# Kernel tuning notes

Hardware: AMD Instinct MI355X
Metric: run time of the kernel (lower is better)

Reference implementation:

```python
import jax, jax.numpy as jnp
import numpy as np

DN = ('NCHW', 'OIHW', 'NCHW')  # conv dimension numbers
EPS = 1e-5


def _tcn(x, w1, b1, w2, b2, w3, b3):
    """Gated TCN. x: [B,T,N,C] -> [B,T-2,N,Cout].  out = conv1(x)*sigmoid(conv2(x)) + tanh(conv3(x))"""
    xc = jnp.transpose(x, (0, 3, 2, 1))  # [B,C,N,T]
    conv = lambda w, b: jax.lax.conv_general_dilated(xc, w, (1, 1), 'VALID', dimension_numbers=DN) + b[None, :, None, None]
    p = conv(w1, b1)
    q = jax.nn.sigmoid(conv(w2, b2))
    r = jnp.tanh(conv(w3, b3))
    out = p * q + r  # [B,Cout,N,T-2]
    return jnp.transpose(out, (0, 3, 2, 1))


def setup_inputs() -> dict:
    key = jax.random.key(0)
    ks = jax.random.split(key, 16)
    B, T, N, C_in = 32, 24, 1024, 1
    K, C_t, C_s = 3, 64, 16
    inp = {}
    inp['x'] = jax.random.normal(ks[0], (B, T, N, C_in), jnp.float32)
    # stacked Chebyshev polynomials T_0..T_{K-1}, scaled so matmul output stays O(1)
    inp['cheb'] = jax.random.normal(ks[1], (K, N, N), jnp.float32) * (N ** -0.5)
    # temporal conv 1 (C_in -> C_t), kernel (1,3)
    s1 = (2.0 / (C_in * 3 + C_t * 3)) ** 0.5
    for i, nm in enumerate(['t1_w1', 't1_w2', 't1_w3']):
        inp[nm] = jax.random.normal(ks[2 + i], (C_t, C_in, 1, 3), jnp.float32) * s1
        inp[nm.replace('w', 'b')] = jnp.zeros((C_t,), jnp.float32)
    # Chebyshev weights (K, C_t, C_s), xavier-normal
    sc = (2.0 / (C_t + C_s)) ** 0.5
    inp['w_cheb'] = jax.random.normal(ks[5], (K, C_t, C_s), jnp.float32) * sc
    inp['b_cheb'] = jnp.zeros((C_s,), jnp.float32)
    # temporal conv 2 (C_s -> C_s)
    s2 = (2.0 / (C_s * 3 + C_s * 3)) ** 0.5
    for i, nm in enumerate(['t2_w1', 't2_w2', 't2_w3']):
        inp[nm] = jax.random.normal(ks[6 + i], (C_s, C_s, 1, 3), jnp.float32) * s2
        inp[nm.replace('w', 'b')] = jnp.zeros((C_s,), jnp.float32)
    # BatchNorm2d over num_nodes channel
    inp['bn_gamma'] = jnp.ones((N,), jnp.float32)
    inp['bn_beta'] = jnp.zeros((N,), jnp.float32)
    return inp


def reference(x, cheb, t1_w1, t1_b1, t1_w2, t1_b2, t1_w3, t1_b3,
              w_cheb, b_cheb, t2_w1, t2_b1, t2_w2, t2_b2, t2_w3, t2_b3,
              bn_gamma, bn_beta):
    # gated TCN 1: [B,24,N,1] -> [B,22,N,64]
    h = _tcn(x, t1_w1, t1_b1, t1_w2, t1_b2, t1_w3, t1_b3)
    # Chebyshev graph conv fused over all time steps and K taps:
    # T_k_x[b,t,n,c] = sum_m h[b,t,m,c] * cheb[k,m,n]; out = sum_k T_k_x @ W[k]
    s = jnp.einsum('btmc,kmn,kco->btno', h, cheb, w_cheb) + b_cheb  # [B,22,N,16]
    # gated TCN 2: -> [B,20,N,16]
    h2 = _tcn(s, t2_w1, t2_b1, t2_w2, t2_b2, t2_w3, t2_b3)
    # BatchNorm2d over node dim (training-mode batch stats), matching permute(0,2,1,3)
    y = jnp.transpose(h2, (0, 2, 1, 3))  # [B,N,T',C]
    mean = jnp.mean(y, axis=(0, 2, 3), keepdims=True)
    var = jnp.var(y, axis=(0, 2, 3), keepdims=True)  # biased, like torch BN
    y = (y - mean) * jax.lax.rsqrt(var + EPS) * bn_gamma[None, :, None, None] + bn_beta[None, :, None, None]
    y = jnp.transpose(y, (0, 2, 1, 3))  # [B,T',N,C]
    return jax.nn.relu(y)
```

## Files before the change

kernel.cpp:

```cpp
#include <hip/hip_runtime.h>
#include <hip/hip_bf16.h>

using bf16x8 = __attribute__((ext_vector_type(8))) short;
using bf16x4 = __attribute__((ext_vector_type(4))) short;
using f32x4  = __attribute__((ext_vector_type(4))) float;
using f32x2  = __attribute__((ext_vector_type(2))) float;

static __device__ __forceinline__ float bf2f(short s) {
  union { unsigned u; float f; } z;
  z.u = ((unsigned)(unsigned short)s) << 16;
  return z.f;
}
static __device__ __forceinline__ short f2bfs(float f) {
  union { __hip_bfloat16 h; short s; } u;
  u.h = __float2bfloat16(f);
  return u.s;
}
static __device__ __forceinline__ float frcp(float x) { return __builtin_amdgcn_rcpf(x); }
static __device__ __forceinline__ float sigm_f(float x) { return frcp(1.f + __expf(-x)); }
static __device__ __forceinline__ float tanh_f(float x) {
  return fmaf(2.f, frcp(1.f + __expf(-2.f * x)), -1.f);
}

typedef const __attribute__((address_space(1))) unsigned int* gas_u32;
typedef __attribute__((address_space(3))) unsigned int* las_u32;
#define GLOAD16(gp, lp) __builtin_amdgcn_global_load_lds( \
    (gas_u32)(const void*)(gp), (las_u32)(void*)(lp), 16, 0, 0)

__global__ void __launch_bounds__(256) k_front(
    const float* __restrict__ x,
    const float* __restrict__ w1, const float* __restrict__ b1,
    const float* __restrict__ w2, const float* __restrict__ b2,
    const float* __restrict__ w3, const float* __restrict__ b3,
    const float* __restrict__ wcheb,
    __hip_bfloat16* __restrict__ hwt, int bt0, int ch,
    const float* __restrict__ cheb, __hip_bfloat16* __restrict__ chebT) {
  __shared__ __align__(16) char smem[32768];
  const int tid = threadIdx.x;

  if ((int)blockIdx.x >= ch * 4) {
    float (*tile)[65] = reinterpret_cast<float (*)[65]>(smem);
    int blk = blockIdx.x - ch * 4;
    int k = blk >> 8;
    int rem = blk & 255;
    int m0 = (rem >> 4) << 6;
    int n0 = (rem & 15) << 6;
    int tx = tid & 63;
    int ty = tid >> 6;
    const float* src = cheb + (size_t)k * 1024 * 1024;
    #pragma unroll
    for (int i = 0; i < 16; i++) {
      int ml = ty + i * 4;
      tile[ml][tx] = src[(size_t)(m0 + ml) * 1024 + n0 + tx];
    }
    __syncthreads();
    #pragma unroll
    for (int i = 0; i < 16; i++) {
      int nl = ty + i * 4;
      chebT[(size_t)(n0 + nl) * 3072 + k * 1024 + m0 + tx] =
          __float2bfloat16(tile[tx][nl]);
    }
    return;
  }

  char* hls = smem;
  const int lane = tid & 63, w = tid >> 6;
  const int r16 = lane & 15, kb = lane >> 4;
  const int btl = blockIdx.x >> 2;
  const int m0 = (blockIdx.x & 3) << 8;
  const int bt = bt0 + btl;
  const int b = bt / 22, t = bt % 22;

  const float* xp = x + (size_t)(b * 24 + t) * 1024 + m0 + tid;
  const float x0 = xp[0], x1 = xp[1024], x2 = xp[2048];
  const f32x2 x0v = {x0, x0}, x1v = {x1, x1}, x2v = {x2, x2};

  bf16x8 bw[3][2];
  #pragma unroll
  for (int kk = 0; kk < 3; kk++)
    #pragma unroll
    for (int ks = 0; ks < 2; ks++)
      #pragma unroll
      for (int jj = 0; jj < 8; jj++)
        bw[kk][ks][jj] = f2bfs(wcheb[kk * 1024 + (ks * 32 + kb * 8 + jj) * 16 + r16]);

  const int rswz = (tid & 7) << 4;
  #pragma unroll
  for (int cg = 0; cg < 8; cg++) {
    bf16x8 hv;
    #pragma unroll
    for (int j2 = 0; j2 < 4; j2++) {
      const int c2 = cg * 4 + j2;
      const int wi = 6 * c2;
      f32x2 pw = {b1[2*c2], b1[2*c2+1]};
      f32x2 qw = {b2[2*c2], b2[2*c2+1]};
      f32x2 rw = {b3[2*c2], b3[2*c2+1]};
      pw = __builtin_elementwise_fma(x0v, (f32x2){w1[wi], w1[wi+3]}, pw);
      qw = __builtin_elementwise_fma(x0v, (f32x2){w2[wi], w2[wi+3]}, qw);
      rw = __builtin_elementwise_fma(x0v, (f32x2){w3[wi], w3[wi+3]}, rw);
      pw = __builtin_elementwise_fma(x1v, (f32x2){w1[wi+1], w1[wi+4]}, pw);
      qw = __builtin_elementwise_fma(x1v, (f32x2){w2[wi+1], w2[wi+4]}, qw);
      rw = __builtin_elementwise_fma(x1v, (f32x2){w3[wi+1], w3[wi+4]}, rw);
      pw = __builtin_elementwise_fma(x2v, (f32x2){w1[wi+2], w1[wi+5]}, pw);
      qw = __builtin_elementwise_fma(x2v, (f32x2){w2[wi+2], w2[wi+5]}, qw);
      rw = __builtin_elementwise_fma(x2v, (f32x2){w3[wi+2], w3[wi+5]}, rw);
      hv[j2*2+0] = f2bfs(fmaf(pw.x, sigm_f(qw.x), tanh_f(rw.x)));
      hv[j2*2+1] = f2bfs(fmaf(pw.y, sigm_f(qw.y), tanh_f(rw.y)));
    }
    *(bf16x8*)(hls + tid * 128 + ((cg << 4) ^ rswz)) = hv;
  }
  __syncthreads();

  const char* Ab = hls + (w * 64 + r16) * 128;
  const int axor = (r16 & 7) << 4;
  f32x4 acc[4][3];
  #pragma unroll
  for (int mt = 0; mt < 4; mt++)
    #pragma unroll
    for (int kk = 0; kk < 3; kk++) acc[mt][kk] = (f32x4){0.f, 0.f, 0.f, 0.f};

  #pragma unroll
  for (int ks = 0; ks < 2; ks++) {
    #pragma unroll
    for (int mt = 0; mt < 4; mt++) {
      bf16x8 a = *(const bf16x8*)(Ab + mt * 2048 + ((((ks << 2) + kb) << 4) ^ axor));
      #pragma unroll
      for (int kk = 0; kk < 3; kk++)
        acc[mt][kk] = __builtin_amdgcn_mfma_f32_16x16x32_bf16(a, bw[kk][ks], acc[mt][kk], 0, 0, 0);
    }
  }

  __hip_bfloat16* hp = hwt + (size_t)btl * 49152 + r16 * 3072 + m0 + w * 64;
  #pragma unroll
  for (int kk = 0; kk < 3; kk++)
    #pragma unroll
    for (int mt = 0; mt < 4; mt++) {
      bf16x4 v;
      #pragma unroll
      for (int r = 0; r < 4; r++) v[r] = f2bfs(acc[mt][kk][r]);
      *(bf16x4*)(hp + kk * 1024 + mt * 16 + kb * 4) = v;
    }
}

__global__ void __launch_bounds__(256, 2) k_gemm(
    const __hip_bfloat16* __restrict__ chebT,
    const __hip_bfloat16* __restrict__ hwt,
    const float* __restrict__ b_cheb,
    __hip_bfloat16* __restrict__ sbuf,
    int bt_base) {
  __shared__ __align__(16) char smem[32768];
  const int tid = threadIdx.x;
  const int lane = tid & 63;
  const int w = tid >> 6;

  int nt, ct;
  if (gridDim.x == 704) {
    const int xcd = blockIdx.x & 7;
    const int idx = blockIdx.x >> 3;
    nt = ((xcd >> 2) << 2) + (idx & 3);
    ct = (xcd & 3) * 22 + (idx >> 2);
  } else {
    nt = blockIdx.x & 7;
    ct = blockIdx.x >> 3;
  }

  const int srow = tid >> 3;
  const int sswz = ((tid & 7) ^ (srow & 7)) << 4;
  const char* Ag = (const char*)chebT + (size_t)(nt * 128 + srow) * 6144 + sswz;
  const int btl = srow >> 4, so = srow & 15;
  const char* Bg = (const char*)hwt + (size_t)(ct * 8 + btl) * 98304 + (size_t)so * 6144 + sswz;
  char* Als = smem + w * 1024;
  char* Bls = smem + 16384 + w * 1024;

  const int r16 = lane & 15;
  const int c16 = lane >> 4;
  const int wr = (w >> 1) << 6;
  const int wc = (w & 1) << 6;
  const int axor = (r16 & 7) << 4;
  const char* Abase = smem + (wr + r16) * 128;
  const char* Bbase = smem + 16384 + (wc + r16) * 128;

  f32x4 acc[4][4];
  #pragma unroll
  for (int i = 0; i < 4; i++)
    #pragma unroll
    for (int j = 0; j < 4; j++) acc[i][j] = (f32x4){0.f, 0.f, 0.f, 0.f};

  for (int kt = 0; kt < 48; kt++) {
    __syncthreads();
    const char* a = Ag + kt * 128;
    const char* b = Bg + kt * 128;
    #pragma unroll
    for (int i = 0; i < 4; i++) GLOAD16(a + i * 196608, Als + i * 4096);
    #pragma unroll
    for (int i = 0; i < 4; i++) GLOAD16(b + i * 196608, Bls + i * 4096);
    __syncthreads();
    #pragma unroll
    for (int ksub = 0; ksub < 2; ksub++) {
      const int ko = (ksub * 64 + c16 * 16) ^ axor;
      bf16x8 af[4], bfr[4];
      #pragma unroll
      for (int i = 0; i < 4; i++) af[i] = *(const bf16x8*)(Abase + i * 2048 + ko);
      #pragma unroll
      for (int j = 0; j < 4; j++) bfr[j] = *(const bf16x8*)(Bbase + j * 2048 + ko);
      #pragma unroll
      for (int i = 0; i < 4; i++)
        #pragma unroll
        for (int j = 0; j < 4; j++)
          acc[i][j] = __builtin_amdgcn_mfma_f32_16x16x32_bf16(af[i], bfr[j], acc[i][j], 0, 0, 0);
    }
  }

  float bias = b_cheb[r16];
  #pragma unroll
  for (int j = 0; j < 4; j++) {
    int gcol = ct * 128 + wc + j * 16 + r16;
    size_t bt_g = (size_t)bt_base + (gcol >> 4);
    int o = gcol & 15;
    #pragma unroll
    for (int i = 0; i < 4; i++) {
      int n0 = nt * 128 + wr + i * 16 + c16 * 4;
      __hip_bfloat16* sp = sbuf + (bt_g * 1024 + n0) * 16 + o;
      #pragma unroll
      for (int r = 0; r < 4; r++)
        sp[r * 16] = __float2bfloat16(acc[i][j][r] + bias);
    }
  }
}

__global__ void __launch_bounds__(256) k_tcn2(
    const __hip_bfloat16* __restrict__ sbuf,
    const float* __restrict__ w1, const float* __restrict__ b1,
    const float* __restrict__ w2, const float* __restrict__ b2,
    const float* __restrict__ w3, const float* __restrict__ b3,
    __hip_bfloat16* __restrict__ h2b) {
  const int tid = threadIdx.x;
  const int lane = tid & 63, w = tid >> 6;
  const int r16 = lane & 15, kb = lane >> 4;
  const int half = blockIdx.x & 1;
  const int bt2 = blockIdx.x >> 1;
  const int b = bt2 / 20, t2 = bt2 % 20;

  bf16x8 bw[3][2];
  const float* wps[3] = {w1, w2, w3};
  #pragma unroll
  for (int c = 0; c < 3; c++) {
    #pragma unroll
    for (int jj = 0; jj < 8; jj++) {
      int k = kb * 8 + jj;
      bw[c][0][jj] = f2bfs(wps[c][r16 * 48 + (k & 15) * 3 + (k >> 4)]);
      bw[c][1][jj] = (kb < 2) ? f2bfs(wps[c][r16 * 48 + (kb * 8 + jj) * 3 + 2]) : (short)0;
    }
  }
  const float bp = b1[r16], bq = b2[r16], br = b3[r16];

  const char* sb = (const char*)sbuf;
  const size_t slice = (size_t)1024 * 32;
  const int rowbase = half * 512 + w * 128;
  const char* baseA = sb + (size_t)(b * 22 + t2 + (kb >> 1)) * slice
                      + (size_t)(rowbase + r16) * 32 + (kb & 1) * 16;
  const char* baseC = sb + (size_t)(b * 22 + t2 + 2) * slice
                      + (size_t)(rowbase + r16) * 32 + (kb & 1) * 16;
  __hip_bfloat16* outp = h2b + ((size_t)bt2 * 1024 + rowbase + kb * 4) * 16 + r16;

  const f32x4 zro = {0.f, 0.f, 0.f, 0.f};
  #pragma unroll 2
  for (int i = 0; i < 8; i++) {
    bf16x8 a0 = *(const bf16x8*)(baseA + i * 512);
    bf16x8 a1{};
    if (kb < 2) a1 = *(const bf16x8*)(baseC + i * 512);
    f32x4 ap = __builtin_amdgcn_mfma_f32_16x16x32_bf16(a0, bw[0][0], zro, 0, 0, 0);
    f32x4 aq = __builtin_amdgcn_mfma_f32_16x16x32_bf16(a0, bw[1][0], zro, 0, 0, 0);
    f32x4 ar = __builtin_amdgcn_mfma_f32_16x16x32_bf16(a0, bw[2][0], zro, 0, 0, 0);
    ap = __builtin_amdgcn_mfma_f32_16x16x32_bf16(a1, bw[0][1], ap, 0, 0, 0);
    aq = __builtin_amdgcn_mfma_f32_16x16x32_bf16(a1, bw[1][1], aq, 0, 0, 0);
    ar = __builtin_amdgcn_mfma_f32_16x16x32_bf16(a1, bw[2][1], ar, 0, 0, 0);
    #pragma unroll
    for (int r = 0; r < 4; r++) {
      float h = fmaf(ap[r] + bp, sigm_f(aq[r] + bq), tanh_f(ar[r] + br));
      outp[(size_t)(i * 16 + r) * 16] = __float2bfloat16(h);
    }
  }
}

__global__ void __launch_bounds__(256) k_stats2(
    const __hip_bfloat16* __restrict__ h2b, float* __restrict__ sums) {
  const int tid = threadIdx.x;
  const int n0 = (blockIdx.x & 7) << 7;
  const int bt2_0 = (blockIdx.x >> 3) << 3;
  const int n = n0 + (tid >> 1);
  const int half = tid & 1;
  const char* base = (const char*)h2b + ((size_t)bt2_0 * 1024 + n) * 32 + half * 16;
  float s = 0.f, s2 = 0.f;
  #pragma unroll
  for (int it = 0; it < 8; it++) {
    bf16x8 v = *(const bf16x8*)(base + (size_t)it * 32768);
    #pragma unroll
    for (int j = 0; j < 8; j++) { float f = bf2f(v[j]); s += f; s2 += f * f; }
  }
  s  += __shfl_xor(s, 1);
  s2 += __shfl_xor(s2, 1);
  if (half == 0) {
    atomicAdd(&sums[n], s);
    atomicAdd(&sums[1024 + n], s2);
  }
}

__global__ void __launch_bounds__(256) k_bnrelu(
    const __hip_bfloat16* __restrict__ h2b, const float* __restrict__ sums,
    const float* __restrict__ gamma, const float* __restrict__ beta,
    float* __restrict__ out) {
  size_t c = (size_t)blockIdx.x * 256 + threadIdx.x;
  int n = (int)((c >> 1) & 1023);
  float S = sums[n], S2 = sums[1024 + n];
  float mean = S * (1.f / 10240.f);
  float var  = S2 * (1.f / 10240.f) - mean * mean;
  float a  = gamma[n] * rsqrtf(var + 1e-5f);
  float cc = beta[n] - mean * a;
  bf16x8 v = *(const bf16x8*)((const char*)h2b + c * 16);
  float4* op = reinterpret_cast<float4*>(out + c * 8);
  float4 o0, o1;
  o0.x = fmaxf(0.f, fmaf(bf2f(v[0]), a, cc));
  o0.y = fmaxf(0.f, fmaf(bf2f(v[1]), a, cc));
  o0.z = fmaxf(0.f, fmaf(bf2f(v[2]), a, cc));
  o0.w = fmaxf(0.f, fmaf(bf2f(v[3]), a, cc));
  o1.x = fmaxf(0.f, fmaf(bf2f(v[4]), a, cc));
  o1.y = fmaxf(0.f, fmaf(bf2f(v[5]), a, cc));
  o1.z = fmaxf(0.f, fmaf(bf2f(v[6]), a, cc));
  o1.w = fmaxf(0.f, fmaf(bf2f(v[7]), a, cc));
  op[0] = o0;
  op[1] = o1;
}

extern "C" void kernel_launch(void* const* d_in, const int* in_sizes, int n_in,
                              void* d_out, int out_size, void* d_ws, size_t ws_size,
                              hipStream_t stream) {
  const float* x     = (const float*)d_in[0];
  const float* cheb  = (const float*)d_in[1];
  const float* t1w1  = (const float*)d_in[2];
  const float* t1b1  = (const float*)d_in[3];
  const float* t1w2  = (const float*)d_in[4];
  const float* t1b2  = (const float*)d_in[5];
  const float* t1w3  = (const float*)d_in[6];
  const float* t1b3  = (const float*)d_in[7];
  const float* wch   = (const float*)d_in[8];
  const float* bch   = (const float*)d_in[9];
  const float* t2w1  = (const float*)d_in[10];
  const float* t2b1  = (const float*)d_in[11];
  const float* t2w2  = (const float*)d_in[12];
  const float* t2b2  = (const float*)d_in[13];
  const float* t2w3  = (const float*)d_in[14];
  const float* t2b3  = (const float*)d_in[15];
  const float* gam   = (const float*)d_in[16];
  const float* bet   = (const float*)d_in[17];

  char* ws = (char*)d_ws;
  __hip_bfloat16* chebT = (__hip_bfloat16*)ws;
  __hip_bfloat16* sbuf  = (__hip_bfloat16*)(ws + 6291456);
  __hip_bfloat16* h2b   = (__hip_bfloat16*)(ws + 29360128);
  float*          sums  = (float*)(ws + 50331648);
  __hip_bfloat16* hwt   = (__hip_bfloat16*)(ws + 50339840);

  size_t avail = ws_size > 50339840 ? ws_size - 50339840 : 0;
  int maxch = (int)(avail / 98304);
  maxch &= ~7;
  if (maxch > 704) maxch = 704;
  if (maxch < 8) maxch = 8;

  hipMemsetAsync(sums, 0, 8192, stream);

  int first = 1;
  for (int bt0 = 0; bt0 < 704; bt0 += maxch) {
    int ch = (704 - bt0 < maxch) ? (704 - bt0) : maxch;
    int extra = first ? 768 : 0;
    k_front<<<ch * 4 + extra, 256, 0, stream>>>(
        x, t1w1, t1b1, t1w2, t1b2, t1w3, t1b3, wch, hwt, bt0, ch, cheb, chebT);
    k_gemm<<<ch, 256, 0, stream>>>(chebT, hwt, bch, sbuf, bt0);
    first = 0;
  }

  k_tcn2<<<1280, 256, 0, stream>>>(sbuf, t2w1, t2b1, t2w2, t2b2, t2w3, t2b3, h2b);
  k_stats2<<<640, 256, 0, stream>>>(h2b, sums);
  k_bnrelu<<<5120, 256, 0, stream>>>(h2b, sums, gam, bet, (float*)d_out);
}
```

Before: 170.4 us.

## Overlap GEMM halves with front and TCN2 work via fused heterogeneous kernels

Splits the 704 batch-time slices into two halves. Combined kernels run the first-half GEMM alongside the second-half front pass, then the second-half GEMM alongside the first-half TCN2. Because independent block types now share one launch, the aim is to fill idle CUs during GEMM tails and remove serialization between stages. The costs are extra launches, mixed register and occupancy limits (launch_bounds 256,2 now applies to the front and TCN2 blocks too), and a more involved fallback path.

Result: slower. 250.7 us (+47.1%).

```diff
diff --git a/kernel.cpp b/kernel.cpp
--- a/kernel.cpp
+++ b/kernel.cpp
@@ -27,47 +27,41 @@
 #define GLOAD16(gp, lp) __builtin_amdgcn_global_load_lds( \
     (gas_u32)(const void*)(gp), (las_u32)(void*)(lp), 16, 0, 0)
 
-__global__ void __launch_bounds__(256) k_front(
+
+static __device__ void dev_transpose(int blk, int tid, char* smem,
+    const float* __restrict__ cheb, __hip_bfloat16* __restrict__ chebT) {
+  float (*tile)[65] = reinterpret_cast<float (*)[65]>(smem);
+  int k = blk >> 8;
+  int rem = blk & 255;
+  int m0 = (rem >> 4) << 6;
+  int n0 = (rem & 15) << 6;
+  int tx = tid & 63;
+  int ty = tid >> 6;
+  const float* src = cheb + (size_t)k * 1024 * 1024;
+  #pragma unroll
+  for (int i = 0; i < 16; i++) {
+    int ml = ty + i * 4;
+    tile[ml][tx] = src[(size_t)(m0 + ml) * 1024 + n0 + tx];
+  }
+  __syncthreads();
+  #pragma unroll
+  for (int i = 0; i < 16; i++) {
+    int nl = ty + i * 4;
+    chebT[(size_t)(n0 + nl) * 3072 + k * 1024 + m0 + tx] =
+        __float2bfloat16(tile[tx][nl]);
+  }
+}
+
+static __device__ void dev_front(int fblk, int bt0, int tid, char* hls,
     const float* __restrict__ x,
     const float* __restrict__ w1, const float* __restrict__ b1,
     const float* __restrict__ w2, const float* __restrict__ b2,
     const float* __restrict__ w3, const float* __restrict__ b3,
-    const float* __restrict__ wcheb,
-    __hip_bfloat16* __restrict__ hwt, int bt0, int ch,
-    const float* __restrict__ cheb, __hip_bfloat16* __restrict__ chebT) {
-  __shared__ __align__(16) char smem[32768];
-  const int tid = threadIdx.x;
-
-  if ((int)blockIdx.x >= ch * 4) {
-    float (*tile)[65] = reinterpret_cast<float (*)[65]>(smem);
-    int blk = blockIdx.x - ch * 4;
-    int k = blk >> 8;
-    int rem = blk & 255;
-    int m0 = (rem >> 4) << 6;
-    int n0 = (rem & 15) << 6;
-    int tx = tid & 63;
-    int ty = tid >> 6;
-    const float* src = cheb + (size_t)k * 1024 * 1024;
-    #pragma unroll
-    for (int i = 0; i < 16; i++) {
-      int ml = ty + i * 4;
-      tile[ml][tx] = src[(size_t)(m0 + ml) * 1024 + n0 + tx];
-    }
-    __syncthreads();
-    #pragma unroll
-    for (int i = 0; i < 16; i++) {
-      int nl = ty + i * 4;
-      chebT[(size_t)(n0 + nl) * 3072 + k * 1024 + m0 + tx] =
-          __float2bfloat16(tile[tx][nl]);
-    }
-    return;
-  }
-
-  char* hls = smem;
+    const float* __restrict__ wcheb, __hip_bfloat16* __restrict__ hwt) {
   const int lane = tid & 63, w = tid >> 6;
   const int r16 = lane & 15, kb = lane >> 4;
-  const int btl = blockIdx.x >> 2;
-  const int m0 = (blockIdx.x & 3) << 8;
+  const int btl = fblk >> 2;
+  const int m0 = (fblk & 3) << 8;
   const int bt = bt0 + btl;
   const int b = bt / 22, t = bt % 22;
 
@@ -130,7 +124,7 @@
     }
   }
 
-  __hip_bfloat16* hp = hwt + (size_t)btl * 49152 + r16 * 3072 + m0 + w * 64;
+  __hip_bfloat16* hp = hwt + (size_t)bt * 49152 + r16 * 3072 + m0 + w * 64;
   #pragma unroll
   for (int kk = 0; kk < 3; kk++)
     #pragma unroll
@@ -142,33 +136,32 @@
     }
 }
 
-__global__ void __launch_bounds__(256, 2) k_gemm(
+static __device__ void dev_gemm(int blk, int ngemm, int bt_base, int tid, char* smem,
     const __hip_bfloat16* __restrict__ chebT,
     const __hip_bfloat16* __restrict__ hwt,
     const float* __restrict__ b_cheb,
-    __hip_bfloat16* __restrict__ sbuf,
-    int bt_base) {
-  __shared__ __align__(16) char smem[32768];
-  const int tid = threadIdx.x;
+    __hip_bfloat16* __restrict__ sbuf) {
   const int lane = tid & 63;
   const int w = tid >> 6;
 
   int nt, ct;
-  if (gridDim.x == 704) {
-    const int xcd = blockIdx.x & 7;
-    const int idx = blockIdx.x >> 3;
+  if ((ngemm & 31) == 0) {
+    const int xcd = blk & 7;
+    const int idx = blk >> 3;
+    const int cgrp = ngemm >> 5;
     nt = ((xcd >> 2) << 2) + (idx & 3);
-    ct = (xcd & 3) * 22 + (idx >> 2);
+    ct = (xcd & 3) * cgrp + (idx >> 2);
   } else {
-    nt = blockIdx.x & 7;
-    ct = blockIdx.x >> 3;
+    nt = blk & 7;
+    ct = blk >> 3;
   }
 
   const int srow = tid >> 3;
   const int sswz = ((tid & 7) ^ (srow & 7)) << 4;
   const char* Ag = (const char*)chebT + (size_t)(nt * 128 + srow) * 6144 + sswz;
   const int btl = srow >> 4, so = srow & 15;
-  const char* Bg = (const char*)hwt + (size_t)(ct * 8 + btl) * 98304 + (size_t)so * 6144 + sswz;
+  const char* Bg = (const char*)hwt + (size_t)(bt_base + ct * 8 + btl) * 98304
+                   + (size_t)so * 6144 + sswz;
   char* Als = smem + w * 1024;
   char* Bls = smem + 16384 + w * 1024;
 
@@ -228,17 +221,16 @@
   }
 }
 
-__global__ void __launch_bounds__(256) k_tcn2(
+static __device__ void dev_tcn2(int idx, int tid,
     const __hip_bfloat16* __restrict__ sbuf,
     const float* __restrict__ w1, const float* __restrict__ b1,
     const float* __restrict__ w2, const float* __restrict__ b2,
     const float* __restrict__ w3, const float* __restrict__ b3,
     __hip_bfloat16* __restrict__ h2b) {
-  const int tid = threadIdx.x;
   const int lane = tid & 63, w = tid >> 6;
   const int r16 = lane & 15, kb = lane >> 4;
-  const int half = blockIdx.x & 1;
-  const int bt2 = blockIdx.x >> 1;
+  const int half = idx & 1;
+  const int bt2 = idx >> 1;
   const int b = bt2 / 20, t2 = bt2 % 20;
 
   bf16x8 bw[3][2];
@@ -281,6 +273,55 @@
       outp[(size_t)(i * 16 + r) * 16] = __float2bfloat16(h);
     }
   }
+}
+
+__global__ void __launch_bounds__(256) k_front(
+    const float* x, const float* w1, const float* b1, const float* w2,
+    const float* b2, const float* w3, const float* b3, const float* wcheb,
+    __hip_bfloat16* hwt, int bt0, int ch,
+    const float* cheb, __hip_bfloat16* chebT) {
+  __shared__ __align__(16) char smem[32768];
+  if ((int)blockIdx.x >= ch * 4)
+    dev_transpose(blockIdx.x - ch * 4, threadIdx.x, smem, cheb, chebT);
+  else
+    dev_front(blockIdx.x, bt0, threadIdx.x, smem,
+              x, w1, b1, w2, b2, w3, b3, wcheb, hwt);
+}
+
+__global__ void __launch_bounds__(256, 2) k_mid(
+    const __hip_bfloat16* chebT, const __hip_bfloat16* hwt_c,
+    const float* bch, __hip_bfloat16* sbuf, int ngemm, int gemm_base,
+    const float* x, const float* w1, const float* b1, const float* w2,
+    const float* b2, const float* w3, const float* b3, const float* wcheb,
+    __hip_bfloat16* hwt, int front_bt0) {
+  __shared__ __align__(16) char smem[32768];
+  if ((int)blockIdx.x < ngemm)
+    dev_gemm(blockIdx.x, ngemm, gemm_base, threadIdx.x, smem,
+             chebT, hwt_c, bch, sbuf);
+  else
+    dev_front(blockIdx.x - ngemm, front_bt0, threadIdx.x, smem,
+              x, w1, b1, w2, b2, w3, b3, wcheb, hwt);
+}
+
+__global__ void __launch_bounds__(256, 2) k_mid2(
+    const __hip_bfloat16* chebT, const __hip_bfloat16* hwt_c,
+    const float* bch, __hip_bfloat16* sbuf, int ngemm, int gemm_base,
+    const float* w1, const float* b1, const float* w2, const float* b2,
+    const float* w3, const float* b3, __hip_bfloat16* h2b) {
+  __shared__ __align__(16) char smem[32768];
+  if ((int)blockIdx.x < ngemm)
+    dev_gemm(blockIdx.x, ngemm, gemm_base, threadIdx.x, smem,
+             chebT, hwt_c, bch, sbuf);
+  else
+    dev_tcn2(blockIdx.x - ngemm, threadIdx.x,
+             sbuf, w1, b1, w2, b2, w3, b3, h2b);
+}
+
+__global__ void __launch_bounds__(256) k_tcn2w(
+    const __hip_bfloat16* sbuf, const float* w1, const float* b1,
+    const float* w2, const float* b2, const float* w3, const float* b3,
+    __hip_bfloat16* h2b, int idx0) {
+  dev_tcn2(blockIdx.x + idx0, threadIdx.x, sbuf, w1, b1, w2, b2, w3, b3, h2b);
 }
 
 __global__ void __launch_bounds__(256) k_stats2(
@@ -361,25 +402,44 @@
   float*          sums  = (float*)(ws + 50331648);
   __hip_bfloat16* hwt   = (__hip_bfloat16*)(ws + 50339840);
 
-  size_t avail = ws_size > 50339840 ? ws_size - 50339840 : 0;
-  int maxch = (int)(avail / 98304);
-  maxch &= ~7;
-  if (maxch > 704) maxch = 704;
-  if (maxch < 8) maxch = 8;
-
+  const size_t need_full = 50339840 + (size_t)704 * 98304;
   hipMemsetAsync(sums, 0, 8192, stream);
 
-  int first = 1;
-  for (int bt0 = 0; bt0 < 704; bt0 += maxch) {
-    int ch = (704 - bt0 < maxch) ? (704 - bt0) : maxch;
-    int extra = first ? 768 : 0;
-    k_front<<<ch * 4 + extra, 256, 0, stream>>>(
-        x, t1w1, t1b1, t1w2, t1b2, t1w3, t1b3, wch, hwt, bt0, ch, cheb, chebT);
-    k_gemm<<<ch, 256, 0, stream>>>(chebT, hwt, bch, sbuf, bt0);
-    first = 0;
-  }
-
-  k_tcn2<<<1280, 256, 0, stream>>>(sbuf, t2w1, t2b1, t2w2, t2b2, t2w3, t2b3, h2b);
-  k_stats2<<<640, 256, 0, stream>>>(h2b, sums);
-  k_bnrelu<<<5120, 256, 0, stream>>>(h2b, sums, gam, bet, (float*)d_out);
-}
+  if (ws_size >= need_full) {
+    const int H = 352;
+    k_front<<<H * 4 + 768, 256, 0, stream>>>(
+        x, t1w1, t1b1, t1w2, t1b2, t1w3, t1b3, wch, hwt, 0, H, cheb, chebT);
+    k_mid<<<H + H * 4, 256, 0, stream>>>(
+        chebT, hwt, bch, sbuf, H, 0,
+        x, t1w1, t1b1, t1w2, t1b2, t1w3, t1b3, wch, hwt, H);
+    k_mid2<<<H + 640, 256, 0, stream>>>(
+        chebT, hwt, bch, sbuf, H, H,
+        t2w1, t2b1, t2w2, t2b2, t2w3, t2b3, h2b);
+    k_tcn2w<<<640, 256, 0, stream>>>(sbuf, t2w1, t2b1, t2w2, t2b2, t2w3, t2b3,
+                                     h2b, 640);
+    k_stats2<<<640, 256, 0, stream>>>(h2b, sums);
+    k_bnrelu<<<5120, 256, 0, stream>>>(h2b, sums, gam, bet, (float*)d_out);
+  } else {
+    size_t avail = ws_size > 50339840 ? ws_size - 50339840 : 0;
+    int maxch = (int)(avail / 98304);
+    maxch &= ~7;
+    if (maxch > 704) maxch = 704;
+    if (maxch < 8) maxch = 8;
+    int first = 1;
+    for (int bt0 = 0; bt0 < 704; bt0 += maxch) {
+      int ch = (704 - bt0 < maxch) ? (704 - bt0) : maxch;
+      int extra = first ? 768 : 0;
+      k_front<<<ch * 4 + extra, 256, 0, stream>>>(
+          x, t1w1, t1b1, t1w2, t1b2, t1w3, t1b3, wch, hwt - (size_t)bt0 * 49152,
+          bt0, ch, cheb, chebT);
+      k_mid<<<ch, 256, 0, stream>>>(
+          chebT, hwt - (size_t)bt0 * 49152, bch, sbuf, ch, bt0,
+          x, t1w1, t1b1, t1w2, t1b2, t1w3, t1b3, wch, hwt, 704 );
+      first = 0;
+    }
+    k_tcn2w<<<1280, 256, 0, stream>>>(sbuf, t2w1, t2b1, t2w2, t2b2, t2w3, t2b3,
+                                      h2b, 0);
+    k_stats2<<<640, 256, 0, stream>>>(h2b, sums);
+    k_bnrelu<<<5120, 256, 0, stream>>>(h2b, sums, gam, bet, (float*)d_out);
+  }
+}
```
